# Kernel tuning notes

Measured on AMD Instinct MI355X. Metric: run time of the kernel, lower is better.

The kernel has to match this reference:

```python
import jax, jax.numpy as jnp
import numpy as np


def _fp_levels(ebits: int, mbits: int) -> np.ndarray:
    """All finite values of an IEEE-like float format (subnormals + normals, single zero)."""
    bias = (1 << (ebits - 1)) - 1
    maxE = (1 << ebits) - 1
    vals = {0.0}
    for sgn in (-1.0, 1.0):
        for F in range(1, 1 << mbits):  # subnormals
            vals.add(sgn * 2.0 ** (1 - bias) * (F / float(1 << mbits)))
        for E in range(1, maxE):  # normals (top exponent excluded: inf/nan)
            for F in range(0, 1 << mbits):
                vals.add(sgn * 2.0 ** (E - bias) * (1.0 + F / float(1 << mbits)))
    return np.array(sorted(vals), dtype=np.float32)


LEVELS_E4M3 = jnp.asarray(_fp_levels(4, 3))  # L = 239 sorted finite levels


def setup_inputs() -> dict:
    key = jax.random.key(0)
    x = jax.random.normal(key, (4096, 8192), dtype=jnp.float32)
    return {"x": x}


def reference(x):
    levels = LEVELS_E4M3.astype(x.dtype)
    L = levels.shape[0]
    max_level = jnp.max(jnp.abs(levels))

    # First forward call: calibrated=False -> ema_maxabs is copied from cur = max|x|.
    # EMA update is under torch.no_grad -> constant w.r.t. x.
    ema = jax.lax.stop_gradient(jnp.max(jnp.abs(x)))
    s = jnp.maximum(ema / (max_level + 1e-12), 1e-8)  # per-tensor scale

    x_scaled = x / s

    # Nearest-level lookup. Equivalent to abs-diff argmin over all L levels, but O(log L)
    # per element via searchsorted on the sorted level table. Ties (exact midpoints)
    # resolve to the LOWER index, matching torch argmin's first-occurrence rule.
    i = jnp.searchsorted(levels, x_scaled)
    lo = jnp.clip(i - 1, 0, L - 1)
    hi = jnp.clip(i, 0, L - 1)
    d_lo = jnp.abs(x_scaled - levels[lo])
    d_hi = jnp.abs(x_scaled - levels[hi])
    idx = jnp.where(d_lo <= d_hi, lo, hi)

    xq = levels[idx] * s
    # STE.forward(xq) == xq + (xq.detach() - xq).detach() == xq in value.
    return xq
```

## Files before the change

### kernel.cpp

```cpp
#include <hip/hip_runtime.h>


#define FP8Q_THREADS 256
#define FP8Q_MAXBLOCKS 2048

__global__ __launch_bounds__(FP8Q_THREADS) void fp8q_absmax_kernel(
    const float4* __restrict__ x4, float* __restrict__ partials,
    const float* __restrict__ x_tail, int n4, int ntail)
{
    int tid = blockIdx.x * blockDim.x + threadIdx.x;
    int stride = gridDim.x * blockDim.x;
    float m = 0.0f;
    for (int i = tid; i < n4; i += stride) {
        float4 v = x4[i];
        m = fmaxf(m, fmaxf(fmaxf(fabsf(v.x), fabsf(v.y)),
                           fmaxf(fabsf(v.z), fabsf(v.w))));
    }
    if (tid < ntail) m = fmaxf(m, fabsf(x_tail[tid]));
    #pragma unroll
    for (int off = 32; off > 0; off >>= 1)
        m = fmaxf(m, __shfl_xor(m, off));
    if ((threadIdx.x & 63) == 0)
        partials[blockIdx.x * (FP8Q_THREADS / 64) + (threadIdx.x >> 6)] = m;
}

__global__ __launch_bounds__(FP8Q_THREADS) void fp8q_reduce_kernel(
    const float* __restrict__ partials, float* __restrict__ scale_out, int np)
{
    __shared__ float smem[FP8Q_THREADS / 64];
    float m = 0.0f;
    for (int i = threadIdx.x; i < np; i += FP8Q_THREADS)
        m = fmaxf(m, partials[i]);
    #pragma unroll
    for (int off = 32; off > 0; off >>= 1)
        m = fmaxf(m, __shfl_xor(m, off));
    if ((threadIdx.x & 63) == 0) smem[threadIdx.x >> 6] = m;
    __syncthreads();
    if (threadIdx.x == 0) {
        float mm = smem[0];
        #pragma unroll
        for (int w = 1; w < FP8Q_THREADS / 64; ++w) mm = fmaxf(mm, smem[w]);
        *scale_out = fmaxf(mm / 240.0f, 1e-8f);
    }
}

__device__ __forceinline__ float fp8q_quant1(float x, float s)
{
    float v = x / s;
    v = fminf(fmaxf(v, -240.0f), 240.0f);
    float m = fabsf(v);
    int e  = (int)(__float_as_uint(m) >> 23) - 127;
    int se = e - 3;
    if (se < -9) se = -9;
    float step     = __uint_as_float((unsigned int)(se + 127) << 23);
    float inv_step = __uint_as_float((unsigned int)(127 - se) << 23);
    float k = v * inv_step;
    float n = ceilf(k - 0.5f);
    return (n * step) * s;
}

__global__ __launch_bounds__(FP8Q_THREADS) void fp8q_quant_kernel(
    const float4* __restrict__ x4, float4* __restrict__ o4,
    const float* __restrict__ x_tail, float* __restrict__ o_tail,
    const float* __restrict__ scale_p, int n4, int ntail)
{
    float s = *scale_p;
    int tid = blockIdx.x * blockDim.x + threadIdx.x;
    int stride = gridDim.x * blockDim.x;
    for (int i = tid; i < n4; i += stride) {
        float4 v = x4[i];
        float4 r;
        r.x = fp8q_quant1(v.x, s);
        r.y = fp8q_quant1(v.y, s);
        r.z = fp8q_quant1(v.z, s);
        r.w = fp8q_quant1(v.w, s);
        o4[i] = r;
    }
    if (tid < ntail) o_tail[tid] = fp8q_quant1(x_tail[tid], s);
}

extern "C" void kernel_launch(void* const* d_in, const int* in_sizes, int n_in,
                              void* d_out, int out_size, void* d_ws, size_t ws_size,
                              hipStream_t stream)
{
    const float* x = (const float*)d_in[0];
    float* out = (float*)d_out;
    int n = in_sizes[0];
    int n4 = n >> 2;
    int ntail = n & 3;
    const float* x_tail = x + (size_t)n4 * 4;
    float* o_tail = out + (size_t)n4 * 4;

    float* scale_p = (float*)d_ws;
    float* partials = (float*)d_ws + 64;

    int blocks = (n4 + FP8Q_THREADS - 1) / FP8Q_THREADS;
    if (blocks > FP8Q_MAXBLOCKS) blocks = FP8Q_MAXBLOCKS;
    if (blocks < 1) blocks = 1;
    int np = blocks * (FP8Q_THREADS / 64);

    fp8q_absmax_kernel<<<blocks, FP8Q_THREADS, 0, stream>>>(
        (const float4*)x, partials, x_tail, n4, ntail);
    fp8q_reduce_kernel<<<1, FP8Q_THREADS, 0, stream>>>(partials, scale_p, np);
    fp8q_quant_kernel<<<blocks, FP8Q_THREADS, 0, stream>>>(
        (const float4*)x, (float4*)out, x_tail, o_tail, scale_p, n4, ntail);
}
```

Baseline: 74.38 us.

## Fold final absmax reduction into quant kernel and use nontemporal stores

Drops the single-block reduce kernel. The absmax kernel now reduces to one partial per block, and every quant block redundantly reduces the 2048 partials to compute the scale itself. This removes one launch and its serialization gap, at the cost of each block reading 8KB of partials. Output stores become nontemporal, to avoid polluting cache with the 128MB write stream.

Result: faster. 68.92 us (-7.3%).

```diff
diff --git a/kernel.cpp b/kernel.cpp
--- a/kernel.cpp
+++ b/kernel.cpp
@@ -1,36 +1,25 @@
 #include <hip/hip_runtime.h>
 
+
+typedef float f32x4 __attribute__((ext_vector_type(4)));
 
 #define FP8Q_THREADS 256
 #define FP8Q_MAXBLOCKS 2048
 
 __global__ __launch_bounds__(FP8Q_THREADS) void fp8q_absmax_kernel(
-    const float4* __restrict__ x4, float* __restrict__ partials,
+    const f32x4* __restrict__ x4, float* __restrict__ partials,
     const float* __restrict__ x_tail, int n4, int ntail)
 {
+    __shared__ float smem[FP8Q_THREADS / 64];
     int tid = blockIdx.x * blockDim.x + threadIdx.x;
     int stride = gridDim.x * blockDim.x;
     float m = 0.0f;
     for (int i = tid; i < n4; i += stride) {
-        float4 v = x4[i];
+        f32x4 v = x4[i];
         m = fmaxf(m, fmaxf(fmaxf(fabsf(v.x), fabsf(v.y)),
                            fmaxf(fabsf(v.z), fabsf(v.w))));
     }
     if (tid < ntail) m = fmaxf(m, fabsf(x_tail[tid]));
-    #pragma unroll
-    for (int off = 32; off > 0; off >>= 1)
-        m = fmaxf(m, __shfl_xor(m, off));
-    if ((threadIdx.x & 63) == 0)
-        partials[blockIdx.x * (FP8Q_THREADS / 64) + (threadIdx.x >> 6)] = m;
-}
-
-__global__ __launch_bounds__(FP8Q_THREADS) void fp8q_reduce_kernel(
-    const float* __restrict__ partials, float* __restrict__ scale_out, int np)
-{
-    __shared__ float smem[FP8Q_THREADS / 64];
-    float m = 0.0f;
-    for (int i = threadIdx.x; i < np; i += FP8Q_THREADS)
-        m = fmaxf(m, partials[i]);
     #pragma unroll
     for (int off = 32; off > 0; off >>= 1)
         m = fmaxf(m, __shfl_xor(m, off));
@@ -40,7 +29,7 @@
         float mm = smem[0];
         #pragma unroll
         for (int w = 1; w < FP8Q_THREADS / 64; ++w) mm = fmaxf(mm, smem[w]);
-        *scale_out = fmaxf(mm / 240.0f, 1e-8f);
+        partials[blockIdx.x] = mm;
     }
 }
 
@@ -60,21 +49,39 @@
 }
 
 __global__ __launch_bounds__(FP8Q_THREADS) void fp8q_quant_kernel(
-    const float4* __restrict__ x4, float4* __restrict__ o4,
+    const f32x4* __restrict__ x4, f32x4* __restrict__ o4,
     const float* __restrict__ x_tail, float* __restrict__ o_tail,
-    const float* __restrict__ scale_p, int n4, int ntail)
+    const float* __restrict__ partials, int np, int n4, int ntail)
 {
-    float s = *scale_p;
+    __shared__ float smem[FP8Q_THREADS / 64];
+    __shared__ float s_shared;
+    float m = 0.0f;
+    for (int i = threadIdx.x; i < np; i += FP8Q_THREADS)
+        m = fmaxf(m, partials[i]);
+    #pragma unroll
+    for (int off = 32; off > 0; off >>= 1)
+        m = fmaxf(m, __shfl_xor(m, off));
+    if ((threadIdx.x & 63) == 0) smem[threadIdx.x >> 6] = m;
+    __syncthreads();
+    if (threadIdx.x == 0) {
+        float mm = smem[0];
+        #pragma unroll
+        for (int w = 1; w < FP8Q_THREADS / 64; ++w) mm = fmaxf(mm, smem[w]);
+        s_shared = fmaxf(mm / 240.0f, 1e-8f);
+    }
+    __syncthreads();
+    float s = s_shared;
+
     int tid = blockIdx.x * blockDim.x + threadIdx.x;
     int stride = gridDim.x * blockDim.x;
     for (int i = tid; i < n4; i += stride) {
-        float4 v = x4[i];
-        float4 r;
+        f32x4 v = x4[i];
+        f32x4 r;
         r.x = fp8q_quant1(v.x, s);
         r.y = fp8q_quant1(v.y, s);
         r.z = fp8q_quant1(v.z, s);
         r.w = fp8q_quant1(v.w, s);
-        o4[i] = r;
+        __builtin_nontemporal_store(r, &o4[i]);
     }
     if (tid < ntail) o_tail[tid] = fp8q_quant1(x_tail[tid], s);
 }
@@ -91,17 +98,14 @@
     const float* x_tail = x + (size_t)n4 * 4;
     float* o_tail = out + (size_t)n4 * 4;
 
-    float* scale_p = (float*)d_ws;
-    float* partials = (float*)d_ws + 64;
+    float* partials = (float*)d_ws;
 
     int blocks = (n4 + FP8Q_THREADS - 1) / FP8Q_THREADS;
     if (blocks > FP8Q_MAXBLOCKS) blocks = FP8Q_MAXBLOCKS;
     if (blocks < 1) blocks = 1;
-    int np = blocks * (FP8Q_THREADS / 64);
 
     fp8q_absmax_kernel<<<blocks, FP8Q_THREADS, 0, stream>>>(
-        (const float4*)x, partials, x_tail, n4, ntail);
-    fp8q_reduce_kernel<<<1, FP8Q_THREADS, 0, stream>>>(partials, scale_p, np);
+        (const f32x4*)x, partials, x_tail, n4, ntail);
     fp8q_quant_kernel<<<blocks, FP8Q_THREADS, 0, stream>>>(
-        (const float4*)x, (float4*)out, x_tail, o_tail, scale_p, n4, ntail);
+        (const f32x4*)x, (f32x4*)out, x_tail, o_tail, partials, blocks, n4, ntail);
 }
```
